# Kernel tuning notes

Measured on AMD Instinct MI355X. Metric: run time of the kernel, lower is better.

The kernel has to match this reference:

```python
import jax, jax.numpy as jnp
import numpy as np

TOP_K = 2

def setup_inputs() -> dict:
    key = jax.random.key(0)
    ks = jax.random.split(key, 5)
    N, D, E, H, O = 2048, 1024, 16, 2048, 1024
    s_in = 1.0 / np.sqrt(D)
    s_h = 1.0 / np.sqrt(H)
    return {
        "z": jax.random.normal(ks[0], (N, D), dtype=jnp.float32),
        "router_w": jax.random.normal(ks[1], (E, D), dtype=jnp.float32) * s_in,
        "router_b": jnp.zeros((E,), dtype=jnp.float32),
        "w1": jax.random.normal(ks[2], (E, H, D), dtype=jnp.float32) * s_in,
        "b1": jnp.zeros((E, H), dtype=jnp.float32),
        "w2": jax.random.normal(ks[3], (E, O, H), dtype=jnp.float32) * s_h,
        "b2": jnp.zeros((E, O), dtype=jnp.float32),
    }

def reference(z, router_w, router_b, w1, b1, w2, b2):
    # Router: softmax over experts, then top-k with renormalized weights
    logits = z @ router_w.T + router_b                      # [N, E]
    probs = jax.nn.softmax(logits, axis=-1)                 # [N, E]
    topk_prob, topk_idx = jax.lax.top_k(probs, TOP_K)       # [N, K]
    topk_prob = topk_prob / topk_prob.sum(axis=-1, keepdims=True)

    # Dense all-expert MLP (faithful to original mix(): every expert on every token)
    h = jax.nn.gelu(jnp.einsum('nd,ehd->neh', z, w1) + b1, approximate=False)  # [N, E, H]
    expert_out = jnp.einsum('neh,eoh->neo', h, w2) + b2                        # [N, E, O]

    # Gather top-k expert outputs and combine with routing weights
    picked = jnp.take_along_axis(expert_out, topk_idx[:, :, None], axis=1)     # [N, K, O]
    return (picked * topk_prob[:, :, None]).sum(axis=1)                        # [N, O]
```

## Files before the change

### kernel.cpp

```cpp
#include <hip/hip_runtime.h>
#include <hip/hip_bf16.h>
#include <math.h>

#define N_TOK 2048
#define DIM   1024
#define NE    16
#define NH    2048
#define NO    1024

typedef __attribute__((ext_vector_type(8))) short short8;
typedef __attribute__((ext_vector_type(4))) float f32x4;

__device__ __forceinline__ unsigned short f2bf(float f) {
  union { float f; unsigned u; } v; v.f = f;
  unsigned r = v.u + 0x7FFFu + ((v.u >> 16) & 1u);
  return (unsigned short)(r >> 16);
}

__device__ __forceinline__ short8 pack8(float4 a, float4 b) {
  short8 r;
  r[0] = (short)f2bf(a.x); r[1] = (short)f2bf(a.y);
  r[2] = (short)f2bf(a.z); r[3] = (short)f2bf(a.w);
  r[4] = (short)f2bf(b.x); r[5] = (short)f2bf(b.y);
  r[6] = (short)f2bf(b.z); r[7] = (short)f2bf(b.w);
  return r;
}

__device__ __forceinline__ unsigned pkbf(float x, float y) {
  float2 f; f.x = x; f.y = y;
  __hip_bfloat162 b = __float22bfloat162_rn(f);
  unsigned u; __builtin_memcpy(&u, &b, 4);
  return u;
}
__device__ __forceinline__ short8 cvt8(float4 a, float4 b) {
  union { short8 s; unsigned u[4]; } r;
  r.u[0] = pkbf(a.x, a.y); r.u[1] = pkbf(a.z, a.w);
  r.u[2] = pkbf(b.x, b.y); r.u[3] = pkbf(b.z, b.w);
  return r.s;
}

__device__ __forceinline__ void glds16(const void* g, void* l) {
  __builtin_amdgcn_global_load_lds(
      (const __attribute__((address_space(1))) void*)g,
      (__attribute__((address_space(3))) void*)l, 16, 0, 0);
}

__device__ __forceinline__ void lds_barrier() {
  __builtin_amdgcn_s_waitcnt(0xC07F);
  __builtin_amdgcn_s_barrier();
}

__global__ __launch_bounds__(256) void router_kernel(
    const float* __restrict__ z, const float* __restrict__ rw,
    const float* __restrict__ rb, int* __restrict__ counts,
    int* __restrict__ list, float* __restrict__ tkw) {
  const int n = blockIdx.x;
  const int t = threadIdx.x;
  const int e = t >> 4, sub = t & 15;
  const float* zr = z + (size_t)n * DIM;
  const float* wr = rw + (size_t)e * DIM;
  double acc = 0.0;
#pragma unroll
  for (int i = 0; i < 16; ++i) {
    const int d = i * 64 + sub * 4;
    const float4 zv = *(const float4*)(zr + d);
    const float4 wv = *(const float4*)(wr + d);
    acc += (double)zv.x * wv.x + (double)zv.y * wv.y
         + (double)zv.z * wv.z + (double)zv.w * wv.w;
  }
  acc += __shfl_xor(acc, 8, 16);
  acc += __shfl_xor(acc, 4, 16);
  acc += __shfl_xor(acc, 2, 16);
  acc += __shfl_xor(acc, 1, 16);
  __shared__ double logits[NE];
  if (sub == 0) logits[e] = acc + (double)rb[e];
  __syncthreads();
  if (t == 0) {
    int i0 = -1, i1 = -1; double v0 = -1e300, v1 = -1e300;
    for (int i = 0; i < NE; ++i) {
      const double v = logits[i];
      if (v > v0) { v1 = v0; i1 = i0; v0 = v; i0 = i; }
      else if (v > v1) { v1 = v; i1 = i; }
    }
    const double w0 = 1.0 / (1.0 + exp(v1 - v0));
    tkw[n * 2 + 0] = (float)w0;
    tkw[n * 2 + 1] = (float)(1.0 - w0);
    const int p0 = atomicAdd(&counts[i0], 1); list[i0 * N_TOK + p0] = n * 2;
    const int p1 = atomicAdd(&counts[i1], 1); list[i1 * N_TOK + p1] = n * 2 + 1;
  }
}

__global__ __launch_bounds__(256) void convert_z_kernel(
    const float* __restrict__ z, unsigned short* __restrict__ zbf) {
  const int i = (blockIdx.x * 256 + threadIdx.x) * 8;
  const float4 a = *(const float4*)(z + i);
  const float4 b = *(const float4*)(z + i + 4);
  *(short8*)(zbf + i) = pack8(a, b);
}

#define BM 64
#define BK 64
#define BN1 128
#define BN2 64
#define NT1 (DIM / BK)
#define NT2 (NH / BK)
#define MT_LEVELS 16
#define GRID_G 4096

__device__ __forceinline__ void decode_bid_xcd(int bid, int& mt, int& e, int& nt) {
  const int slot = bid >> 3;
  e = (bid & 7) + ((slot & 1) << 3);
  mt = (slot >> 1) & 15;
  nt = slot >> 5;
}

__global__ __launch_bounds__(256, 3) void gemm1_kernel(
    const unsigned short* __restrict__ zbf, const float* __restrict__ w1,
    const float* __restrict__ b1, const int* __restrict__ counts,
    const int* __restrict__ list, unsigned short* __restrict__ h) {
  int mt, e, nt;
  decode_bid_xcd(blockIdx.x, mt, e, nt);
  const int ne = counts[e];
  if (mt * BM >= ne) return;
  const int t = threadIdx.x;

  __shared__ __align__(16) unsigned char As[BM * BK * 2];
  __shared__ __align__(16) unsigned char Bs[BN1 * BK * 4];
  __shared__ int ent_s[BM];
  if (t < BM) {
    const int idx = mt * BM + t;
    ent_s[t] = (idx < ne) ? list[e * N_TOK + idx] : -1;
  }
  __syncthreads();

  const int lane = t & 63, w = t >> 6;
  const unsigned short* aP[2];
  const float* bP[8];
  unsigned char *aL[2], *bL[8];
  {
    const int l3 = lane >> 3, c7 = lane & 7;
#pragma unroll
    for (int p = 0; p < 2; ++p) {
      const int CI = w + 4 * p;
      const int R = 8 * CI + l3;
      const int c = c7 ^ (R & 7);
      const int en = ent_s[R];
      aP[p] = zbf + (size_t)(en >= 0 ? (en >> 1) : 0) * DIM + c * 8;
      aL[p] = As + CI * 1024;
    }
    const int l4 = lane >> 4, c15 = lane & 15;
    const float* bbase = w1 + ((size_t)e * NH + (size_t)nt * BN1) * DIM;
#pragma unroll
    for (int q = 0; q < 8; ++q) {
      const int CI = w + 4 * q;
      const int R = 4 * CI + l4;
      const int c = c15 ^ (R & 15);
      bP[q] = bbase + (size_t)R * DIM + c * 4;
      bL[q] = Bs + CI * 1024;
    }
  }

  const int wm = (w & 1) * 32, wn = (w >> 1) * 64;
  const int l15 = lane & 15, quad = lane >> 4;

  f32x4 acc[2][4];
#pragma unroll
  for (int i = 0; i < 2; ++i)
#pragma unroll
    for (int j = 0; j < 4; ++j) acc[i][j] = (f32x4){0.f, 0.f, 0.f, 0.f};

  for (int k0 = 0; k0 < DIM; k0 += BK) {
#pragma unroll
    for (int p = 0; p < 2; ++p) glds16(aP[p] + k0, aL[p]);
#pragma unroll
    for (int q = 0; q < 8; ++q) glds16(bP[q] + k0, bL[q]);
    __syncthreads();
#pragma unroll
    for (int kk = 0; kk < BK; kk += 32) {
      short8 af[2], bfr[4];
#pragma unroll
      for (int i = 0; i < 2; ++i) {
        const int R = wm + i * 16 + l15;
        const int c0 = (kk >> 3) + quad;
        af[i] = *(const short8*)(As + R * 128 + ((c0 ^ (R & 7)) << 4));
      }
#pragma unroll
      for (int j = 0; j < 4; ++j) {
        const int R = wn + j * 16 + l15;
        const int c0 = (kk >> 2) + 2 * quad;
        const float4 f0 = *(const float4*)(Bs + R * 256 + ((c0 ^ (R & 15)) << 4));
        const float4 f1 = *(const float4*)(Bs + R * 256 + (((c0 + 1) ^ (R & 15)) << 4));
        bfr[j] = cvt8(f0, f1);
      }
#pragma unroll
      for (int i = 0; i < 2; ++i)
#pragma unroll
        for (int j = 0; j < 4; ++j)
          acc[i][j] = __builtin_amdgcn_mfma_f32_16x16x32_bf16(af[i], bfr[j], acc[i][j], 0, 0, 0);
    }
    lds_barrier();
  }

  const int r4 = quad * 4;
#pragma unroll
  for (int i = 0; i < 2; ++i) {
#pragma unroll
    for (int reg = 0; reg < 4; ++reg) {
      const int row = wm + i * 16 + r4 + reg;
      const int en = ent_s[row];
      if (en < 0) continue;
      unsigned short* hrow = h + (size_t)en * NH;
#pragma unroll
      for (int j = 0; j < 4; ++j) {
        const int col = nt * BN1 + wn + j * 16 + l15;
        float v = acc[i][j][reg] + b1[e * NH + col];
        v = 0.5f * v * (1.0f + erff(v * 0.70710678118654752f));
        hrow[col] = f2bf(v);
      }
    }
  }
}

__global__ __launch_bounds__(256, 4) void gemm2_kernel(
    const unsigned short* __restrict__ h, const float* __restrict__ w2,
    const float* __restrict__ b2, const int* __restrict__ counts,
    const int* __restrict__ list, const float* __restrict__ tkw,
    float* __restrict__ out) {
  int mt, e, nt;
  decode_bid_xcd(blockIdx.x, mt, e, nt);
  const int ne = counts[e];
  if (mt * BM >= ne) return;
  const int t = threadIdx.x;

  __shared__ __align__(16) unsigned char As[BM * BK * 2];
  __shared__ __align__(16) unsigned char Bs[BN2 * BK * 4];
  __shared__ int ent_s[BM];
  if (t < BM) {
    const int idx = mt * BM + t;
    ent_s[t] = (idx < ne) ? list[e * N_TOK + idx] : -1;
  }
  __syncthreads();

  const int lane = t & 63, w = t >> 6;
  const unsigned short* aP[2];
  const float* bP[4];
  unsigned char *aL[2], *bL[4];
  {
    const int l3 = lane >> 3, c7 = lane & 7;
#pragma unroll
    for (int p = 0; p < 2; ++p) {
      const int CI = w + 4 * p;
      const int R = 8 * CI + l3;
      const int c = c7 ^ (R & 7);
      const int en = ent_s[R];
      aP[p] = h + (size_t)(en >= 0 ? en : 0) * NH + c * 8;
      aL[p] = As + CI * 1024;
    }
    const int l4 = lane >> 4, c15 = lane & 15;
    const float* bbase = w2 + ((size_t)e * NO + (size_t)nt * BN2) * NH;
#pragma unroll
    for (int q = 0; q < 4; ++q) {
      const int CI = w + 4 * q;
      const int R = 4 * CI + l4;
      const int c = c15 ^ (R & 15);
      bP[q] = bbase + (size_t)R * NH + c * 4;
      bL[q] = Bs + CI * 1024;
    }
  }

  const int wm = (w & 1) * 32, wn = (w >> 1) * 32;
  const int l15 = lane & 15, quad = lane >> 4;

  f32x4 acc[2][2];
#pragma unroll
  for (int i = 0; i < 2; ++i)
#pragma unroll
    for (int j = 0; j < 2; ++j) acc[i][j] = (f32x4){0.f, 0.f, 0.f, 0.f};

  for (int k0 = 0; k0 < NH; k0 += BK) {
#pragma unroll
    for (int p = 0; p < 2; ++p) glds16(aP[p] + k0, aL[p]);
#pragma unroll
    for (int q = 0; q < 4; ++q) glds16(bP[q] + k0, bL[q]);
    __syncthreads();
#pragma unroll
    for (int kk = 0; kk < BK; kk += 32) {
      short8 af[2], bfr[2];
#pragma unroll
      for (int i = 0; i < 2; ++i) {
        const int R = wm + i * 16 + l15;
        const int c0 = (kk >> 3) + quad;
        af[i] = *(const short8*)(As + R * 128 + ((c0 ^ (R & 7)) << 4));
      }
#pragma unroll
      for (int j = 0; j < 2; ++j) {
        const int R = wn + j * 16 + l15;
        const int c0 = (kk >> 2) + 2 * quad;
        const float4 f0 = *(const float4*)(Bs + R * 256 + ((c0 ^ (R & 15)) << 4));
        const float4 f1 = *(const float4*)(Bs + R * 256 + (((c0 + 1) ^ (R & 15)) << 4));
        bfr[j] = cvt8(f0, f1);
      }
#pragma unroll
      for (int i = 0; i < 2; ++i)
#pragma unroll
        for (int j = 0; j < 2; ++j)
          acc[i][j] = __builtin_amdgcn_mfma_f32_16x16x32_bf16(af[i], bfr[j], acc[i][j], 0, 0, 0);
    }
    lds_barrier();
  }

  const int r4 = quad * 4;
#pragma unroll
  for (int i = 0; i < 2; ++i) {
#pragma unroll
    for (int reg = 0; reg < 4; ++reg) {
      const int row = wm + i * 16 + r4 + reg;
      const int en = ent_s[row];
      if (en < 0) continue;
      const float wgt = tkw[en];
      float* orow = out + (size_t)(en >> 1) * NO;
#pragma unroll
      for (int j = 0; j < 2; ++j) {
        const int col = nt * BN2 + wn + j * 16 + l15;
        atomicAdd(&orow[col], wgt * (acc[i][j][reg] + b2[e * NO + col]));
      }
    }
  }
}

extern "C" void kernel_launch(void* const* d_in, const int* in_sizes, int n_in,
                              void* d_out, int out_size, void* d_ws, size_t ws_size,
                              hipStream_t stream) {
  const float* z  = (const float*)d_in[0];
  const float* rw = (const float*)d_in[1];
  const float* rb = (const float*)d_in[2];
  const float* w1 = (const float*)d_in[3];
  const float* b1 = (const float*)d_in[4];
  const float* w2 = (const float*)d_in[5];
  const float* b2 = (const float*)d_in[6];
  float* out = (float*)d_out;

  char* ws = (char*)d_ws;
  int*   counts = (int*)ws;
  int*   list   = (int*)(ws + 256);
  float* tkw    = (float*)(ws + 256 + 131072);
  unsigned short* zbf = (unsigned short*)(ws + 262144);
  unsigned short* h = (unsigned short*)(ws + 262144 + 4194304);

  hipMemsetAsync(counts, 0, NE * sizeof(int), stream);
  hipMemsetAsync(out, 0, (size_t)N_TOK * NO * sizeof(float), stream);
  convert_z_kernel<<<(N_TOK * DIM / 8) / 256, 256, 0, stream>>>(z, zbf);
  router_kernel<<<N_TOK, 256, 0, stream>>>(z, rw, rb, counts, list, tkw);
  gemm1_kernel<<<GRID_G, 256, 0, stream>>>(zbf, w1, b1, counts, list, h);
  gemm2_kernel<<<GRID_G, 256, 0, stream>>>(h, w2, b2, counts, list, tkw, out);
}
```

Measured before the change: 478.5 us.

## Pre-convert expert weights to bf16, register-load B, double-buffer A, split-K gemm2

Adds a pass that converts w1 and w2 to bf16 in the workspace on every call. The two expert GEMMs then load weight fragments straight from global memory into registers, so the fp32 LDS staging and per-fragment conversion go away. The A tiles grow to 128 rows and are double-buffered in LDS with prefetch of the next k-step, and gemm2 is split into two K halves that both add into the output with atomics. This trades an extra read-convert-write pass over all weights for halving weight traffic and conversion work inside the GEMMs. The new block mapping covers at most 1024 routed entries per expert, so heavier routing imbalance than that would drop rows.

```diff
diff --git a/kernel.cpp b/kernel.cpp
--- a/kernel.cpp
+++ b/kernel.cpp
@@ -43,11 +43,6 @@
   __builtin_amdgcn_global_load_lds(
       (const __attribute__((address_space(1))) void*)g,
       (__attribute__((address_space(3))) void*)l, 16, 0, 0);
-}
-
-__device__ __forceinline__ void lds_barrier() {
-  __builtin_amdgcn_s_waitcnt(0xC07F);
-  __builtin_amdgcn_s_barrier();
 }
 
 __global__ __launch_bounds__(256) void router_kernel(
@@ -98,34 +93,73 @@
   *(short8*)(zbf + i) = pack8(a, b);
 }
 
-#define BM 64
+__global__ __launch_bounds__(256) void convert_w_kernel(
+    const float* __restrict__ src, unsigned short* __restrict__ dst) {
+  const size_t i = ((size_t)blockIdx.x * 256 + threadIdx.x) * 8;
+  const float4 a = *(const float4*)(src + i);
+  const float4 b = *(const float4*)(src + i + 4);
+  *(short8*)(dst + i) = cvt8(a, b);
+}
+
+#define BM 128
 #define BK 64
-#define BN1 128
-#define BN2 64
-#define NT1 (DIM / BK)
-#define NT2 (NH / BK)
-#define MT_LEVELS 16
-#define GRID_G 4096
-
-__device__ __forceinline__ void decode_bid_xcd(int bid, int& mt, int& e, int& nt) {
-  const int slot = bid >> 3;
-  e = (bid & 7) + ((slot & 1) << 3);
-  mt = (slot >> 1) & 15;
-  nt = slot >> 5;
-}
+#define BN 64
+#define ASZ (BM * BK * 2)
+
+#define GSTEP(KT, NSTEP, BU, BN_)                                          \
+  {                                                                        \
+    if ((KT) + 1 < (NSTEP)) {                                              \
+      const int k1 = ((KT) + 1) * BK;                                      \
+      _Pragma("unroll")                                                    \
+      for (int p = 0; p < 4; ++p)                                          \
+        glds16(aP[p] + k1, aL[p] + (((KT) + 1) & 1) * ASZ);                \
+      _Pragma("unroll")                                                    \
+      for (int j = 0; j < 2; ++j) {                                        \
+        BN_[j * 2 + 0] = *(const short8*)(bRow[j] + k1);                   \
+        BN_[j * 2 + 1] = *(const short8*)(bRow[j] + k1 + 32);              \
+      }                                                                    \
+    }                                                                      \
+    const unsigned char* Ac = As + ((KT) & 1) * ASZ;                       \
+    _Pragma("unroll")                                                      \
+    for (int kk2 = 0; kk2 < 2; ++kk2) {                                    \
+      short8 af[4];                                                        \
+      const int c0 = kk2 * 4 + quad;                                       \
+      _Pragma("unroll")                                                    \
+      for (int i = 0; i < 4; ++i) {                                        \
+        const int R = wm + i * 16 + l15;                                   \
+        af[i] = *(const short8*)(Ac + R * 128 + ((c0 ^ (R & 7)) << 4));    \
+      }                                                                    \
+      _Pragma("unroll")                                                    \
+      for (int i = 0; i < 4; ++i)                                          \
+        _Pragma("unroll")                                                  \
+        for (int j = 0; j < 2; ++j)                                        \
+          acc[i][j] = __builtin_amdgcn_mfma_f32_16x16x32_bf16(             \
+              af[i], BU[j * 2 + kk2], acc[i][j], 0, 0, 0);                 \
+    }                                                                      \
+    __syncthreads();                                                       \
+  }
 
 __global__ __launch_bounds__(256, 3) void gemm1_kernel(
-    const unsigned short* __restrict__ zbf, const float* __restrict__ w1,
+    const unsigned short* __restrict__ zbf, const unsigned short* __restrict__ w1b,
     const float* __restrict__ b1, const int* __restrict__ counts,
     const int* __restrict__ list, unsigned short* __restrict__ h) {
+  const int bid = blockIdx.x;
   int mt, e, nt;
-  decode_bid_xcd(blockIdx.x, mt, e, nt);
+  if (bid < 1024) {
+    mt = bid & 1;
+    const int rest = bid >> 1;
+    e = rest & 15; nt = rest >> 4;
+  } else {
+    const int t2 = bid - 1024;
+    mt = 2 + (t2 >> 9);
+    const int r = t2 & 511;
+    e = r & 15; nt = r >> 4;
+  }
   const int ne = counts[e];
   if (mt * BM >= ne) return;
   const int t = threadIdx.x;
 
-  __shared__ __align__(16) unsigned char As[BM * BK * 2];
-  __shared__ __align__(16) unsigned char Bs[BN1 * BK * 4];
+  __shared__ __align__(16) unsigned char As[2 * ASZ];
   __shared__ int ent_s[BM];
   if (t < BM) {
     const int idx = mt * BM + t;
@@ -134,13 +168,12 @@
   __syncthreads();
 
   const int lane = t & 63, w = t >> 6;
-  const unsigned short* aP[2];
-  const float* bP[8];
-  unsigned char *aL[2], *bL[8];
+  const unsigned short* aP[4];
+  unsigned char* aL[4];
   {
     const int l3 = lane >> 3, c7 = lane & 7;
 #pragma unroll
-    for (int p = 0; p < 2; ++p) {
+    for (int p = 0; p < 4; ++p) {
       const int CI = w + 4 * p;
       const int R = 8 * CI + l3;
       const int c = c7 ^ (R & 7);
@@ -148,62 +181,39 @@
       aP[p] = zbf + (size_t)(en >= 0 ? (en >> 1) : 0) * DIM + c * 8;
       aL[p] = As + CI * 1024;
     }
-    const int l4 = lane >> 4, c15 = lane & 15;
-    const float* bbase = w1 + ((size_t)e * NH + (size_t)nt * BN1) * DIM;
-#pragma unroll
-    for (int q = 0; q < 8; ++q) {
-      const int CI = w + 4 * q;
-      const int R = 4 * CI + l4;
-      const int c = c15 ^ (R & 15);
-      bP[q] = bbase + (size_t)R * DIM + c * 4;
-      bL[q] = Bs + CI * 1024;
-    }
-  }
-
-  const int wm = (w & 1) * 32, wn = (w >> 1) * 64;
+  }
+  const int wm = (w & 1) * 64, wn = (w >> 1) * 32;
   const int l15 = lane & 15, quad = lane >> 4;
 
-  f32x4 acc[2][4];
-#pragma unroll
-  for (int i = 0; i < 2; ++i)
-#pragma unroll
-    for (int j = 0; j < 4; ++j) acc[i][j] = (f32x4){0.f, 0.f, 0.f, 0.f};
-
-  for (int k0 = 0; k0 < DIM; k0 += BK) {
-#pragma unroll
-    for (int p = 0; p < 2; ++p) glds16(aP[p] + k0, aL[p]);
-#pragma unroll
-    for (int q = 0; q < 8; ++q) glds16(bP[q] + k0, bL[q]);
-    __syncthreads();
-#pragma unroll
-    for (int kk = 0; kk < BK; kk += 32) {
-      short8 af[2], bfr[4];
-#pragma unroll
-      for (int i = 0; i < 2; ++i) {
-        const int R = wm + i * 16 + l15;
-        const int c0 = (kk >> 3) + quad;
-        af[i] = *(const short8*)(As + R * 128 + ((c0 ^ (R & 7)) << 4));
-      }
-#pragma unroll
-      for (int j = 0; j < 4; ++j) {
-        const int R = wn + j * 16 + l15;
-        const int c0 = (kk >> 2) + 2 * quad;
-        const float4 f0 = *(const float4*)(Bs + R * 256 + ((c0 ^ (R & 15)) << 4));
-        const float4 f1 = *(const float4*)(Bs + R * 256 + (((c0 + 1) ^ (R & 15)) << 4));
-        bfr[j] = cvt8(f0, f1);
-      }
-#pragma unroll
-      for (int i = 0; i < 2; ++i)
-#pragma unroll
-        for (int j = 0; j < 4; ++j)
-          acc[i][j] = __builtin_amdgcn_mfma_f32_16x16x32_bf16(af[i], bfr[j], acc[i][j], 0, 0, 0);
-    }
-    lds_barrier();
+  const unsigned short* bRow[2];
+#pragma unroll
+  for (int j = 0; j < 2; ++j)
+    bRow[j] = w1b + ((size_t)e * NH + (size_t)(nt * BN + wn + j * 16 + l15)) * DIM + quad * 8;
+
+  f32x4 acc[4][2];
+#pragma unroll
+  for (int i = 0; i < 4; ++i)
+#pragma unroll
+    for (int j = 0; j < 2; ++j) acc[i][j] = (f32x4){0.f, 0.f, 0.f, 0.f};
+
+  short8 bA[4], bB[4];
+#pragma unroll
+  for (int p = 0; p < 4; ++p) glds16(aP[p], aL[p]);
+#pragma unroll
+  for (int j = 0; j < 2; ++j) {
+    bA[j * 2 + 0] = *(const short8*)(bRow[j]);
+    bA[j * 2 + 1] = *(const short8*)(bRow[j] + 32);
+  }
+  __syncthreads();
+
+  for (int kt2 = 0; kt2 < 8; ++kt2) {
+    GSTEP(kt2 * 2,     16, bA, bB);
+    GSTEP(kt2 * 2 + 1, 16, bB, bA);
   }
 
   const int r4 = quad * 4;
 #pragma unroll
-  for (int i = 0; i < 2; ++i) {
+  for (int i = 0; i < 4; ++i) {
 #pragma unroll
     for (int reg = 0; reg < 4; ++reg) {
       const int row = wm + i * 16 + r4 + reg;
@@ -211,8 +221,8 @@
       if (en < 0) continue;
       unsigned short* hrow = h + (size_t)en * NH;
 #pragma unroll
-      for (int j = 0; j < 4; ++j) {
-        const int col = nt * BN1 + wn + j * 16 + l15;
+      for (int j = 0; j < 2; ++j) {
+        const int col = nt * BN + wn + j * 16 + l15;
         float v = acc[i][j][reg] + b1[e * NH + col];
         v = 0.5f * v * (1.0f + erff(v * 0.70710678118654752f));
         hrow[col] = f2bf(v);
@@ -221,19 +231,30 @@
   }
 }
 
-__global__ __launch_bounds__(256, 4) void gemm2_kernel(
-    const unsigned short* __restrict__ h, const float* __restrict__ w2,
+__global__ __launch_bounds__(256, 3) void gemm2_kernel(
+    const unsigned short* __restrict__ h, const unsigned short* __restrict__ w2b,
     const float* __restrict__ b2, const int* __restrict__ counts,
     const int* __restrict__ list, const float* __restrict__ tkw,
     float* __restrict__ out) {
-  int mt, e, nt;
-  decode_bid_xcd(blockIdx.x, mt, e, nt);
+  const int bid = blockIdx.x;
+  int mt, e, nt, ks;
+  if (bid < 1024) {
+    mt = bid & 1;
+    ks = (bid >> 1) & 1;
+    const int rest = bid >> 2;
+    e = rest & 15; nt = rest >> 4;
+  } else {
+    const int t2 = bid - 1024;
+    mt = 2 + (t2 >> 9);
+    const int r = t2 & 511;
+    ks = r & 1; e = (r >> 1) & 15; nt = r >> 5;
+  }
   const int ne = counts[e];
   if (mt * BM >= ne) return;
   const int t = threadIdx.x;
-
-  __shared__ __align__(16) unsigned char As[BM * BK * 2];
-  __shared__ __align__(16) unsigned char Bs[BN2 * BK * 4];
+  const int kbase = ks * (NH / 2);
+
+  __shared__ __align__(16) unsigned char As[2 * ASZ];
   __shared__ int ent_s[BM];
   if (t < BM) {
     const int idx = mt * BM + t;
@@ -242,76 +263,52 @@
   __syncthreads();
 
   const int lane = t & 63, w = t >> 6;
-  const unsigned short* aP[2];
-  const float* bP[4];
-  unsigned char *aL[2], *bL[4];
+  const unsigned short* aP[4];
+  unsigned char* aL[4];
   {
     const int l3 = lane >> 3, c7 = lane & 7;
 #pragma unroll
-    for (int p = 0; p < 2; ++p) {
+    for (int p = 0; p < 4; ++p) {
       const int CI = w + 4 * p;
       const int R = 8 * CI + l3;
       const int c = c7 ^ (R & 7);
       const int en = ent_s[R];
-      aP[p] = h + (size_t)(en >= 0 ? en : 0) * NH + c * 8;
+      aP[p] = h + (size_t)(en >= 0 ? en : 0) * NH + kbase + c * 8;
       aL[p] = As + CI * 1024;
     }
-    const int l4 = lane >> 4, c15 = lane & 15;
-    const float* bbase = w2 + ((size_t)e * NO + (size_t)nt * BN2) * NH;
-#pragma unroll
-    for (int q = 0; q < 4; ++q) {
-      const int CI = w + 4 * q;
-      const int R = 4 * CI + l4;
-      const int c = c15 ^ (R & 15);
-      bP[q] = bbase + (size_t)R * NH + c * 4;
-      bL[q] = Bs + CI * 1024;
-    }
-  }
-
-  const int wm = (w & 1) * 32, wn = (w >> 1) * 32;
+  }
+  const int wm = (w & 1) * 64, wn = (w >> 1) * 32;
   const int l15 = lane & 15, quad = lane >> 4;
 
-  f32x4 acc[2][2];
-#pragma unroll
-  for (int i = 0; i < 2; ++i)
+  const unsigned short* bRow[2];
+#pragma unroll
+  for (int j = 0; j < 2; ++j)
+    bRow[j] = w2b + ((size_t)e * NO + (size_t)(nt * BN + wn + j * 16 + l15)) * NH + kbase + quad * 8;
+
+  f32x4 acc[4][2];
+#pragma unroll
+  for (int i = 0; i < 4; ++i)
 #pragma unroll
     for (int j = 0; j < 2; ++j) acc[i][j] = (f32x4){0.f, 0.f, 0.f, 0.f};
 
-  for (int k0 = 0; k0 < NH; k0 += BK) {
-#pragma unroll
-    for (int p = 0; p < 2; ++p) glds16(aP[p] + k0, aL[p]);
-#pragma unroll
-    for (int q = 0; q < 4; ++q) glds16(bP[q] + k0, bL[q]);
-    __syncthreads();
-#pragma unroll
-    for (int kk = 0; kk < BK; kk += 32) {
-      short8 af[2], bfr[2];
-#pragma unroll
-      for (int i = 0; i < 2; ++i) {
-        const int R = wm + i * 16 + l15;
-        const int c0 = (kk >> 3) + quad;
-        af[i] = *(const short8*)(As + R * 128 + ((c0 ^ (R & 7)) << 4));
-      }
-#pragma unroll
-      for (int j = 0; j < 2; ++j) {
-        const int R = wn + j * 16 + l15;
-        const int c0 = (kk >> 2) + 2 * quad;
-        const float4 f0 = *(const float4*)(Bs + R * 256 + ((c0 ^ (R & 15)) << 4));
-        const float4 f1 = *(const float4*)(Bs + R * 256 + (((c0 + 1) ^ (R & 15)) << 4));
-        bfr[j] = cvt8(f0, f1);
-      }
-#pragma unroll
-      for (int i = 0; i < 2; ++i)
-#pragma unroll
-        for (int j = 0; j < 2; ++j)
-          acc[i][j] = __builtin_amdgcn_mfma_f32_16x16x32_bf16(af[i], bfr[j], acc[i][j], 0, 0, 0);
-    }
-    lds_barrier();
+  short8 bA[4], bB[4];
+#pragma unroll
+  for (int p = 0; p < 4; ++p) glds16(aP[p], aL[p]);
+#pragma unroll
+  for (int j = 0; j < 2; ++j) {
+    bA[j * 2 + 0] = *(const short8*)(bRow[j]);
+    bA[j * 2 + 1] = *(const short8*)(bRow[j] + 32);
+  }
+  __syncthreads();
+
+  for (int kt2 = 0; kt2 < 8; ++kt2) {
+    GSTEP(kt2 * 2,     16, bA, bB);
+    GSTEP(kt2 * 2 + 1, 16, bB, bA);
   }
 
   const int r4 = quad * 4;
 #pragma unroll
-  for (int i = 0; i < 2; ++i) {
+  for (int i = 0; i < 4; ++i) {
 #pragma unroll
     for (int reg = 0; reg < 4; ++reg) {
       const int row = wm + i * 16 + r4 + reg;
@@ -321,8 +318,10 @@
       float* orow = out + (size_t)(en >> 1) * NO;
 #pragma unroll
       for (int j = 0; j < 2; ++j) {
-        const int col = nt * BN2 + wn + j * 16 + l15;
-        atomicAdd(&orow[col], wgt * (acc[i][j][reg] + b2[e * NO + col]));
+        const int col = nt * BN + wn + j * 16 + l15;
+        float v = wgt * acc[i][j][reg];
+        if (ks == 0) v += wgt * b2[e * NO + col];
+        atomicAdd(&orow[col], v);
       }
     }
   }
@@ -346,11 +345,16 @@
   float* tkw    = (float*)(ws + 256 + 131072);
   unsigned short* zbf = (unsigned short*)(ws + 262144);
   unsigned short* h = (unsigned short*)(ws + 262144 + 4194304);
+  const size_t base = 262144 + 4194304 + 16777216;
+  unsigned short* w1b = (unsigned short*)(ws + base);
+  unsigned short* w2b = (unsigned short*)(ws + base + (size_t)NE * NH * DIM * 2);
 
   hipMemsetAsync(counts, 0, NE * sizeof(int), stream);
   hipMemsetAsync(out, 0, (size_t)N_TOK * NO * sizeof(float), stream);
   convert_z_kernel<<<(N_TOK * DIM / 8) / 256, 256, 0, stream>>>(z, zbf);
   router_kernel<<<N_TOK, 256, 0, stream>>>(z, rw, rb, counts, list, tkw);
-  gemm1_kernel<<<GRID_G, 256, 0, stream>>>(zbf, w1, b1, counts, list, h);
-  gemm2_kernel<<<GRID_G, 256, 0, stream>>>(h, w2, b2, counts, list, tkw, out);
-}
+  convert_w_kernel<<<(int)(((size_t)NE * NH * DIM / 8) / 256), 256, 0, stream>>>(w1, w1b);
+  convert_w_kernel<<<(int)(((size_t)NE * NO * NH / 8) / 256), 256, 0, stream>>>(w2, w2b);
+  gemm1_kernel<<<4096, 256, 0, stream>>>(zbf, w1b, b1, counts, list, h);
+  gemm2_kernel<<<4096, 256, 0, stream>>>(h, w2b, b2, counts, list, tkw, out);
+}
```

Result: slower. 530.8 us (+10.9%).
